# Optimization experiments

Measured on AMD Instinct MI355X. Metric: run time of the kernel, lower is better.

The kernel has to match this reference:

```python
import jax, jax.numpy as jnp
import numpy as np


def _chamfer(pred, tgt):
    # pred: [B,N,3], tgt: [B,M,3]
    # Euclidean pairwise distances (same math as torch.cdist, p=2)
    p2 = jnp.sum(pred * pred, axis=-1)              # [B,N]
    t2 = jnp.sum(tgt * tgt, axis=-1)                # [B,M]
    cross = jnp.einsum('bnd,bmd->bnm', pred, tgt)   # [B,N,M]
    sq = p2[:, :, None] + t2[:, None, :] - 2.0 * cross
    dist = jnp.sqrt(jnp.maximum(sq, 0.0))           # [B,N,M]
    min_p2t = jnp.min(dist, axis=2)                 # [B,N]
    min_t2p = jnp.min(dist, axis=1)                 # [B,M]
    return jnp.mean(min_p2t) + jnp.mean(min_t2p)


def setup_inputs() -> dict:
    key = jax.random.key(0)
    k1, k2 = jax.random.split(key)
    B, N, M, D = 8, 4096, 4096, 3
    predicted_points = jax.random.normal(k1, (B, N, D), dtype=jnp.float32)
    target_points = jax.random.normal(k2, (B, M, D), dtype=jnp.float32)
    return {"predicted_points": predicted_points, "target_points": target_points}


def reference(predicted_points, target_points):
    return _chamfer(predicted_points, target_points)
```

## Files before the change

### kernel.cpp

```cpp
#include <hip/hip_runtime.h>
#include <math.h>

#define B_SZ 8
#define N_SZ 4096
#define M_SZ 4096
#define NQ (B_SZ * N_SZ)
#define TOT (2 * NQ)

#define BQ 128
#define BT 128
#define NIG (N_SZ / BQ)
#define NJG (M_SZ / BT)
#define NG  32

#define NBLK2 (TOT / 256)


__device__ __forceinline__ float min3f(float a, float b, float c) {
    float d;
    asm("v_min3_f32 %0, %1, %2, %3" : "=v"(d) : "v"(a), "v"(b), "v"(c));
    return d;
}

__global__ __launch_bounds__(256)
void chamfer_cross_kernel(const float* __restrict__ pred,
                          const float* __restrict__ tgt,
                          float* __restrict__ part)
{
    const int b  = blockIdx.z;
    const int ig = blockIdx.y;
    const int jg = blockIdx.x;

    __shared__ float4 sq[BQ];
    __shared__ float4 st[BT];
    __shared__ float  redR[BQ][17];
    __shared__ float  redC[BT][17];

    {
        const int k = threadIdx.x;
        if (k < BQ) {
            const float* s = pred + ((size_t)b * N_SZ + ig * BQ + k) * 3;
            float x = s[0], y = s[1], z = s[2];
            sq[k] = make_float4(x, y, z, 0.5f * (x * x + y * y + z * z));
        } else {
            const int k2 = k - BQ;
            const float* s = tgt + ((size_t)b * M_SZ + jg * BT + k2) * 3;
            float x = s[0], y = s[1], z = s[2];
            st[k2] = make_float4(x, y, z, 0.5f * (x * x + y * y + z * z));
        }
    }
    __syncthreads();

    const int r = threadIdx.x >> 4;
    const int c = threadIdx.x & 15;

    float qxn[8], qyn[8], qzn[8], hq[8];
    float tx[8], ty[8], tz[8], ht[8];
#pragma unroll
    for (int i = 0; i < 8; ++i) {
        float4 v = sq[r * 8 + i];
        qxn[i] = -v.x; qyn[i] = -v.y; qzn[i] = -v.z; hq[i] = v.w;
    }
#pragma unroll
    for (int j = 0; j < 8; ++j) {
        float4 v = st[c * 8 + j];
        tx[j] = v.x; ty[j] = v.y; tz[j] = v.z; ht[j] = v.w;
    }

    float mr[8], mc[8];
#pragma unroll
    for (int i = 0; i < 8; ++i) { mr[i] = 3.0e38f; mc[i] = 3.0e38f; }

#pragma unroll
    for (int j = 0; j < 8; j += 2) {
#pragma unroll
        for (int i = 0; i < 8; i += 2) {
            float r00 = fmaf(qxn[i],     tx[j],     ht[j]);
            r00 = fmaf(qyn[i],     ty[j],     r00);
            r00 = fmaf(qzn[i],     tz[j],     r00);
            float r01 = fmaf(qxn[i],     tx[j + 1], ht[j + 1]);
            r01 = fmaf(qyn[i],     ty[j + 1], r01);
            r01 = fmaf(qzn[i],     tz[j + 1], r01);
            float r10 = fmaf(qxn[i + 1], tx[j],     ht[j]);
            r10 = fmaf(qyn[i + 1], ty[j],     r10);
            r10 = fmaf(qzn[i + 1], tz[j],     r10);
            float r11 = fmaf(qxn[i + 1], tx[j + 1], ht[j + 1]);
            r11 = fmaf(qyn[i + 1], ty[j + 1], r11);
            r11 = fmaf(qzn[i + 1], tz[j + 1], r11);
            mr[i]     = min3f(mr[i],     r00, r01);
            mr[i + 1] = min3f(mr[i + 1], r10, r11);
            float c00 = r00 + hq[i];
            float c10 = r10 + hq[i + 1];
            mc[j]     = min3f(mc[j],     c00, c10);
            float c01 = r01 + hq[i];
            float c11 = r11 + hq[i + 1];
            mc[j + 1] = min3f(mc[j + 1], c01, c11);
        }
    }

#pragma unroll
    for (int i = 0; i < 8; ++i) redR[r * 8 + i][c] = mr[i] + hq[i];
#pragma unroll
    for (int j = 0; j < 8; ++j) redC[c * 8 + j][r] = mc[j];
    __syncthreads();

    const int tid = threadIdx.x;
    if (tid < BQ) {
        float m = 3.0e38f;
#pragma unroll
        for (int k = 0; k < 16; ++k) m = fminf(m, redR[tid][k]);
        part[(size_t)jg * TOT + (size_t)b * N_SZ + ig * BQ + tid] = m;
    } else {
        const int t = tid - BQ;
        float m = 3.0e38f;
#pragma unroll
        for (int k = 0; k < 16; ++k) m = fminf(m, redC[t][k]);
        part[(size_t)ig * TOT + NQ + (size_t)b * M_SZ + jg * BT + t] = m;
    }
}

__global__ __launch_bounds__(256)
void chamfer_combine_kernel(const float* __restrict__ part,
                            float* __restrict__ bsum)
{
    const int q = blockIdx.x * 256 + threadIdx.x;
    float m = 3.0e38f;
#pragma unroll
    for (int g = 0; g < NG; ++g) m = fminf(m, part[(size_t)g * TOT + q]);
    float d = sqrtf(2.0f * fmaxf(m, 0.0f));
#pragma unroll
    for (int off = 32; off > 0; off >>= 1) d += __shfl_down(d, off);
    __shared__ float rs[4];
    if ((threadIdx.x & 63) == 0) rs[threadIdx.x >> 6] = d;
    __syncthreads();
    if (threadIdx.x == 0) bsum[blockIdx.x] = rs[0] + rs[1] + rs[2] + rs[3];
}

__global__ __launch_bounds__(64)
void chamfer_final_kernel(const float* __restrict__ bsum,
                          float* __restrict__ out)
{
    float s = 0.0f;
#pragma unroll
    for (int i = 0; i < NBLK2 / 64; ++i) s += bsum[threadIdx.x + i * 64];
#pragma unroll
    for (int off = 32; off > 0; off >>= 1) s += __shfl_down(s, off);
    if (threadIdx.x == 0) out[0] = s * (1.0f / (float)NQ);
}

extern "C" void kernel_launch(void* const* d_in, const int* in_sizes, int n_in,
                              void* d_out, int out_size, void* d_ws, size_t ws_size,
                              hipStream_t stream) {
    const float* pred = (const float*)d_in[0];
    const float* tgt  = (const float*)d_in[1];
    float* out = (float*)d_out;

    float* part = (float*)d_ws;
    float* bsum = part + (size_t)NG * TOT;

    dim3 grid1(NJG, NIG, B_SZ);
    chamfer_cross_kernel<<<grid1, 256, 0, stream>>>(pred, tgt, part);
    chamfer_combine_kernel<<<NBLK2, 256, 0, stream>>>(part, bsum);
    chamfer_final_kernel<<<1, 64, 0, stream>>>(bsum, out);
}
```

Before: 86.81 us.

## Enlarge cross-distance tiles to 256x256 with 16x16 per-thread register blocking

Doubles the query and target tile sizes so each thread computes a 16x16 block of distances instead of 8x8. This cuts the number of partial-min slices from 32 to 16, which halves the partial buffer written by the cross kernel and read by the combine kernel, and raises arithmetic per shared-memory load. The row and column reductions now share one shared-memory array with extra barriers. The cost is much higher register pressure per thread and a quarter as many blocks, which may reduce occupancy or cause spills.

Result: faster. 84.13 us (-3.1%).

```diff
diff --git a/kernel.cpp b/kernel.cpp
--- a/kernel.cpp
+++ b/kernel.cpp
@@ -7,11 +7,11 @@
 #define NQ (B_SZ * N_SZ)
 #define TOT (2 * NQ)
 
-#define BQ 128
-#define BT 128
+#define BQ 256
+#define BT 256
 #define NIG (N_SZ / BQ)
 #define NJG (M_SZ / BT)
-#define NG  32
+#define NG  16
 
 #define NBLK2 (TOT / 256)
 
@@ -30,51 +30,46 @@
     const int b  = blockIdx.z;
     const int ig = blockIdx.y;
     const int jg = blockIdx.x;
+    const int tid = threadIdx.x;
 
     __shared__ float4 sq[BQ];
     __shared__ float4 st[BT];
-    __shared__ float  redR[BQ][17];
-    __shared__ float  redC[BT][17];
+    __shared__ float  red[256][17];
 
     {
-        const int k = threadIdx.x;
-        if (k < BQ) {
-            const float* s = pred + ((size_t)b * N_SZ + ig * BQ + k) * 3;
-            float x = s[0], y = s[1], z = s[2];
-            sq[k] = make_float4(x, y, z, 0.5f * (x * x + y * y + z * z));
-        } else {
-            const int k2 = k - BQ;
-            const float* s = tgt + ((size_t)b * M_SZ + jg * BT + k2) * 3;
-            float x = s[0], y = s[1], z = s[2];
-            st[k2] = make_float4(x, y, z, 0.5f * (x * x + y * y + z * z));
-        }
+        const float* sp = pred + ((size_t)b * N_SZ + ig * BQ + tid) * 3;
+        float x = sp[0], y = sp[1], z = sp[2];
+        sq[tid] = make_float4(x, y, z, 0.5f * (x * x + y * y + z * z));
+        const float* sv = tgt + ((size_t)b * M_SZ + jg * BT + tid) * 3;
+        x = sv[0]; y = sv[1]; z = sv[2];
+        st[tid] = make_float4(x, y, z, 0.5f * (x * x + y * y + z * z));
     }
     __syncthreads();
 
-    const int r = threadIdx.x >> 4;
-    const int c = threadIdx.x & 15;
+    const int r = tid >> 4;
+    const int c = tid & 15;
 
-    float qxn[8], qyn[8], qzn[8], hq[8];
-    float tx[8], ty[8], tz[8], ht[8];
+    float qxn[16], qyn[16], qzn[16], hq[16];
+    float tx[16], ty[16], tz[16], ht[16];
 #pragma unroll
-    for (int i = 0; i < 8; ++i) {
-        float4 v = sq[r * 8 + i];
+    for (int i = 0; i < 16; ++i) {
+        float4 v = sq[r * 16 + i];
         qxn[i] = -v.x; qyn[i] = -v.y; qzn[i] = -v.z; hq[i] = v.w;
     }
 #pragma unroll
-    for (int j = 0; j < 8; ++j) {
-        float4 v = st[c * 8 + j];
+    for (int j = 0; j < 16; ++j) {
+        float4 v = st[c * 16 + j];
         tx[j] = v.x; ty[j] = v.y; tz[j] = v.z; ht[j] = v.w;
     }
 
-    float mr[8], mc[8];
+    float mr[16], mc[16];
 #pragma unroll
-    for (int i = 0; i < 8; ++i) { mr[i] = 3.0e38f; mc[i] = 3.0e38f; }
+    for (int i = 0; i < 16; ++i) { mr[i] = 3.0e38f; mc[i] = 3.0e38f; }
 
 #pragma unroll
-    for (int j = 0; j < 8; j += 2) {
+    for (int j = 0; j < 16; j += 2) {
 #pragma unroll
-        for (int i = 0; i < 8; i += 2) {
+        for (int i = 0; i < 16; i += 2) {
             float r00 = fmaf(qxn[i],     tx[j],     ht[j]);
             r00 = fmaf(qyn[i],     ty[j],     r00);
             r00 = fmaf(qzn[i],     tz[j],     r00);
@@ -99,23 +94,24 @@
     }
 
 #pragma unroll
-    for (int i = 0; i < 8; ++i) redR[r * 8 + i][c] = mr[i] + hq[i];
+    for (int i = 0; i < 16; ++i) red[r * 16 + i][c] = mr[i] + hq[i];
+    __syncthreads();
+    {
+        float m = 3.0e38f;
 #pragma unroll
-    for (int j = 0; j < 8; ++j) redC[c * 8 + j][r] = mc[j];
+        for (int k = 0; k < 16; k += 2) m = min3f(m, red[tid][k], red[tid][k + 1]);
+        part[(size_t)jg * TOT + (size_t)b * N_SZ + ig * BQ + tid] = m;
+    }
     __syncthreads();
 
-    const int tid = threadIdx.x;
-    if (tid < BQ) {
+#pragma unroll
+    for (int j = 0; j < 16; ++j) red[c * 16 + j][r] = mc[j];
+    __syncthreads();
+    {
         float m = 3.0e38f;
 #pragma unroll
-        for (int k = 0; k < 16; ++k) m = fminf(m, redR[tid][k]);
-        part[(size_t)jg * TOT + (size_t)b * N_SZ + ig * BQ + tid] = m;
-    } else {
-        const int t = tid - BQ;
-        float m = 3.0e38f;
-#pragma unroll
-        for (int k = 0; k < 16; ++k) m = fminf(m, redC[t][k]);
-        part[(size_t)ig * TOT + NQ + (size_t)b * M_SZ + jg * BT + t] = m;
+        for (int k = 0; k < 16; k += 2) m = min3f(m, red[tid][k], red[tid][k + 1]);
+        part[(size_t)ig * TOT + NQ + (size_t)b * M_SZ + jg * BT + tid] = m;
     }
 }
 
```
